# Optimization experiments

Hardware: AMD Instinct MI355X
Metric: run time of the kernel (lower is better)

The kernel has to match this reference:

```python
import jax, jax.numpy as jnp
import numpy as np
import math

EMBED_DIM = 1024
N_HEADS = 16
HEAD_DIM = EMBED_DIM // N_HEADS
B, N = 2, 2048


def setup_inputs() -> dict:
    key = jax.random.key(0)
    k1, k2, k3 = jax.random.split(key, 3)
    x = jax.random.normal(k1, (B, N, EMBED_DIM), dtype=jnp.float32)
    # Per-head Linear(D, 3*head_dim), stacked over heads. PyTorch Linear init scale ~1/sqrt(fan_in).
    bound = 1.0 / math.sqrt(EMBED_DIM)
    Wkqv = jax.random.uniform(k2, (N_HEADS, EMBED_DIM, 3 * HEAD_DIM), dtype=jnp.float32, minval=-bound, maxval=bound)
    bkqv = jax.random.uniform(k3, (N_HEADS, 3 * HEAD_DIM), dtype=jnp.float32, minval=-bound, maxval=bound)
    return {"x": x, "Wkqv": Wkqv, "bkqv": bkqv}


def reference(x, Wkqv, bkqv):
    Bx, Nx, D = x.shape
    hd = Wkqv.shape[-1] // 3
    # all heads at once: [B, H, N, 3*hd]
    proj = jnp.einsum('bnd,hdf->bhnf', x, Wkqv) + bkqv[None, :, None, :]
    # torch.split order in the original is (k, q, v)
    k, q, v = jnp.split(proj, 3, axis=-1)
    # scores = q @ k^T / sqrt(head_dim)   [B, H, N, N]
    scores = jnp.einsum('bhqd,bhkd->bhqk', q, k) / math.sqrt(hd)
    causal = jnp.tril(jnp.ones((Nx, Nx), dtype=bool))
    scores = jnp.where(causal[None, None, :, :], scores, -jnp.inf)
    attn = jax.nn.softmax(scores, axis=-1)
    out = jnp.einsum('bhqk,bhkd->bhqd', attn, v)  # [B, H, N, hd]
    # concat heads -> [B, N, D]  (forward() passes no out_matrix, so no output projection)
    return out.transpose(0, 2, 1, 3).reshape(Bx, Nx, D)
```

## Files before the change

### kernel.cpp

```cpp
#include <hip/hip_runtime.h>
#include <math.h>

typedef float f32x4 __attribute__((ext_vector_type(4)));
typedef __bf16 bf16x8 __attribute__((ext_vector_type(8)));
typedef __bf16 bf16x4 __attribute__((ext_vector_type(4)));

#define MFMA16(a, b, c) __builtin_amdgcn_mfma_f32_16x16x32_bf16((a), (b), (c), 0, 0, 0)

constexpr int Bsz = 2, Nseq = 2048, Dm = 1024, Hh = 16, HDim = 64, F3 = 192;
constexpr int Mrows = Bsz * Nseq;
constexpr int NC = Hh * F3;
constexpr float QSCALE = 0.125f * 1.4426950408889634f;

__device__ inline void load_lds16(const void* g, void* l) {
    __builtin_amdgcn_global_load_lds((const __attribute__((address_space(1))) void*)g,
                                     (__attribute__((address_space(3))) void*)l, 16, 0, 0);
}

#define FENCE asm volatile("" ::: "memory")
#define BARRIER do { FENCE; __builtin_amdgcn_s_barrier(); FENCE; } while (0)


__global__ __launch_bounds__(256) void conv_xw_kernel(const float* __restrict__ x,
                                                      __bf16* __restrict__ xb,
                                                      const float* __restrict__ w,
                                                      __bf16* __restrict__ wt) {
    __shared__ __bf16 tile[32][66];
    if (blockIdx.x < 2048) {
        int i = blockIdx.x * 256 + threadIdx.x;
        const float4* xv = reinterpret_cast<const float4*>(x);
        float4 a = xv[2 * i];
        float4 b = xv[2 * i + 1];
        bf16x8 o = {(__bf16)a.x, (__bf16)a.y, (__bf16)a.z, (__bf16)a.w,
                    (__bf16)b.x, (__bf16)b.y, (__bf16)b.z, (__bf16)b.w};
        *reinterpret_cast<bf16x8*>(xb + 8 * i) = o;
    } else {
        int id = blockIdx.x - 2048;
        int h = id / 96, rem = id % 96;
        int d0 = (rem & 31) * 32, c0 = (rem >> 5) * 64;
        for (int i = threadIdx.x; i < 32 * 64; i += 256) {
            int di = i >> 6, cj = i & 63;
            tile[di][cj] = (__bf16)w[(size_t)(h * Dm + d0 + di) * F3 + c0 + cj];
        }
        __syncthreads();
        for (int i = threadIdx.x; i < 32 * 64; i += 256) {
            int ci = i >> 5, dj = i & 31;
            wt[(size_t)(h * F3 + c0 + ci) * Dm + d0 + dj] = tile[dj][ci];
        }
    }
}

__global__ __launch_bounds__(256) void conv_w_kernel(const float* __restrict__ w,
                                                     __bf16* __restrict__ wt) {
    __shared__ __bf16 tile[32][66];
    int h = blockIdx.z, d0 = blockIdx.x * 32, c0 = blockIdx.y * 64;
    for (int i = threadIdx.x; i < 32 * 64; i += 256) {
        int di = i >> 6, cj = i & 63;
        tile[di][cj] = (__bf16)w[(size_t)(h * Dm + d0 + di) * F3 + c0 + cj];
    }
    __syncthreads();
    for (int i = threadIdx.x; i < 32 * 64; i += 256) {
        int ci = i >> 5, dj = i & 31;
        wt[(size_t)(h * F3 + c0 + ci) * Dm + d0 + dj] = tile[dj][ci];
    }
}

__global__ __launch_bounds__(512, 2) void gemm_proj(const __bf16* __restrict__ xb,
                                                    const __bf16* __restrict__ wt,
                                                    const float* __restrict__ bias,
                                                    __bf16* __restrict__ kbuf,
                                                    __bf16* __restrict__ qbuf,
                                                    __bf16* __restrict__ vt) {
    __shared__ __align__(16) __bf16 Ab[2][256 * 64];
    __shared__ __align__(16) __bf16 Bb[2][192 * 64];

    int flat = blockIdx.x;
    int swz = (flat & 7) * 32 + (flat >> 3);
    int bm = swz >> 4, bn = swz & 15;
    int r0 = bm * 256, n0 = bn * 192;

    int w = threadIdx.x >> 6, lane = threadIdx.x & 63;
    int col = lane & 15, quad = lane >> 4;
    int wm = w >> 2, wn = w & 3;

    f32x4 acc[8][3] = {};

    int rl = lane >> 3;
    int cg = ((lane & 7) ^ rl) * 8;

    auto stage = [&](int t, int s) {
#pragma unroll
        for (int i = 0; i < 4; i++) {
            int rowb = w * 32 + i * 8;
            load_lds16(xb + (size_t)(r0 + rowb + rl) * Dm + t * 64 + cg,
                       &Ab[s][rowb * 64]);
        }
#pragma unroll
        for (int i = 0; i < 3; i++) {
            int rowb = w * 24 + i * 8;
            load_lds16(wt + (size_t)(n0 + rowb + rl) * Dm + t * 64 + cg,
                       &Bb[s][rowb * 64]);
        }
    };

    stage(0, 0);
    stage(1, 1);

    for (int j = 0; j < 16; j++) {
        int s = j & 1;
        if (j < 15) asm volatile("s_waitcnt vmcnt(7)" ::: "memory");
        else        asm volatile("s_waitcnt vmcnt(0)" ::: "memory");
        BARRIER;

#pragma unroll
        for (int ks = 0; ks < 2; ks++) {
            int cq = ks * 4 + quad;
            bf16x8 af[8], bfr[3];
#pragma unroll
            for (int mt = 0; mt < 8; mt++) {
                int row = wm * 128 + mt * 16 + col;
                af[mt] = *reinterpret_cast<const bf16x8*>(
                    &Ab[s][row * 64 + ((cq ^ (row & 7)) * 8)]);
            }
#pragma unroll
            for (int nt = 0; nt < 3; nt++) {
                int row = wn * 48 + nt * 16 + col;
                bfr[nt] = *reinterpret_cast<const bf16x8*>(
                    &Bb[s][row * 64 + ((cq ^ (row & 7)) * 8)]);
            }
            __builtin_amdgcn_s_setprio(1);
#pragma unroll
            for (int mt = 0; mt < 8; mt++)
#pragma unroll
                for (int nt = 0; nt < 3; nt++)
                    acc[mt][nt] = MFMA16(af[mt], bfr[nt], acc[mt][nt]);
            __builtin_amdgcn_s_setprio(0);
        }

        BARRIER;
        if (j + 2 < 16) stage(j + 2, s);
    }

#pragma unroll
    for (int nt = 0; nt < 3; nt++) {
        int g = n0 + wn * 48 + nt * 16 + col;
        int h = g / F3, c = g - h * F3;
        float bv = bias[g];
        bool isq = (c >= 64 && c < 128), isv = (c >= 128);
        int cd = c & 63;
#pragma unroll
        for (int mt = 0; mt < 8; mt++) {
#pragma unroll
            for (int rg = 0; rg < 4; rg++) {
                int r = r0 + wm * 128 + mt * 16 + quad * 4 + rg;
                int b = r >> 11, n = r & (Nseq - 1);
                float v = acc[mt][nt][rg] + bv;
                if (isq) v *= QSCALE;
                size_t bh = (size_t)(b * Hh + h);
                if (isv) {
                    int np = (n & ~63) | ((n & 15) << 2) | ((n >> 4) & 3);
                    vt[(bh * HDim + cd) * Nseq + np] = (__bf16)v;
                } else {
                    ((isq) ? qbuf : kbuf)[(bh * Nseq + n) * HDim + cd] = (__bf16)v;
                }
            }
        }
    }
}

__global__ __launch_bounds__(256) void proj_small(const float* __restrict__ x,
                                                  const __bf16* __restrict__ wt,
                                                  const float* __restrict__ bias,
                                                  __bf16* __restrict__ kbuf,
                                                  __bf16* __restrict__ qbuf,
                                                  __bf16* __restrict__ vt) {
    int h = blockIdx.y;
    int wave = threadIdx.x >> 6, lane = threadIdx.x & 63;
    int col = lane & 15, quad = lane >> 4;
    int r0 = blockIdx.x * 128 + wave * 32;

    f32x4 acc[12][2] = {};
    const float* xr0 = x + (size_t)(r0 + col) * Dm + quad * 8;
    const float* xr1 = xr0 + 16 * Dm;
    const __bf16* wbase = wt + (size_t)(h * F3 + col) * Dm + quad * 8;

    for (int k0 = 0; k0 < Dm; k0 += 32) {
        float4 a0lo = *reinterpret_cast<const float4*>(xr0 + k0);
        float4 a0hi = *reinterpret_cast<const float4*>(xr0 + k0 + 4);
        float4 a1lo = *reinterpret_cast<const float4*>(xr1 + k0);
        float4 a1hi = *reinterpret_cast<const float4*>(xr1 + k0 + 4);
        bf16x8 a0 = {(__bf16)a0lo.x, (__bf16)a0lo.y, (__bf16)a0lo.z, (__bf16)a0lo.w,
                     (__bf16)a0hi.x, (__bf16)a0hi.y, (__bf16)a0hi.z, (__bf16)a0hi.w};
        bf16x8 a1 = {(__bf16)a1lo.x, (__bf16)a1lo.y, (__bf16)a1lo.z, (__bf16)a1lo.w,
                     (__bf16)a1hi.x, (__bf16)a1hi.y, (__bf16)a1hi.z, (__bf16)a1hi.w};
#pragma unroll
        for (int ct = 0; ct < 12; ct++) {
            bf16x8 bf = *reinterpret_cast<const bf16x8*>(wbase + ct * 16 * Dm + k0);
            acc[ct][0] = MFMA16(a0, bf, acc[ct][0]);
            acc[ct][1] = MFMA16(a1, bf, acc[ct][1]);
        }
    }
#pragma unroll
    for (int ct = 0; ct < 12; ct++) {
        int c = ct * 16 + col;
        float bv = bias[h * F3 + c];
        int cd = c & 63;
        bool isq = (c >= 64 && c < 128), isv = (c >= 128);
#pragma unroll
        for (int rt = 0; rt < 2; rt++) {
#pragma unroll
            for (int rg = 0; rg < 4; rg++) {
                int r = r0 + rt * 16 + quad * 4 + rg;
                int b = r >> 11, n = r & (Nseq - 1);
                float v = acc[ct][rt][rg] + bv;
                if (isq) v *= QSCALE;
                size_t bh = (size_t)(b * Hh + h);
                if (isv) {
                    int np = (n & ~63) | ((n & 15) << 2) | ((n >> 4) & 3);
                    vt[(bh * HDim + cd) * Nseq + np] = (__bf16)v;
                } else {
                    ((isq) ? qbuf : kbuf)[(bh * Nseq + n) * HDim + cd] = (__bf16)v;
                }
            }
        }
    }
}

__global__ __launch_bounds__(256) void attn_kernel(const __bf16* __restrict__ qbuf,
                                                   const __bf16* __restrict__ kbuf,
                                                   const __bf16* __restrict__ vt,
                                                   float* __restrict__ out) {
    __shared__ __align__(16) __bf16 Kb[2][64 * 64];
    __shared__ __align__(16) __bf16 Vb[2][64 * 64];
    __shared__ __align__(16) __bf16 plds[4][16 * 64];
    int bh = blockIdx.x;
    int b = bh >> 4, h = bh & 15;
    int tile = 31 - blockIdx.y;
    int wave = threadIdx.x >> 6, lane = threadIdx.x & 63;
    int col = lane & 15, quad = lane >> 4;
    int q0 = tile * 64 + wave * 16;

    const __bf16* qbase = qbuf + (size_t)bh * Nseq * HDim;
    const __bf16* kbase = kbuf + (size_t)bh * Nseq * HDim;
    const __bf16* vbase = vt + (size_t)bh * HDim * Nseq;

    bf16x8 aq0 = *reinterpret_cast<const bf16x8*>(qbase + (q0 + col) * HDim + quad * 8);
    bf16x8 aq1 = *reinterpret_cast<const bf16x8*>(qbase + (q0 + col) * HDim + quad * 8 + 32);

    const bf16x8 vone = {(__bf16)1.f, (__bf16)1.f, (__bf16)1.f, (__bf16)1.f,
                         (__bf16)1.f, (__bf16)1.f, (__bf16)1.f, (__bf16)1.f};

    f32x4 o[4] = {};
    f32x4 ls = {};

    int mb = tile * 64;
    int loop_end = mb + 64;

    int rl = lane >> 3;
    int srow0 = wave * 16 + rl;
    int srow1 = wave * 16 + 8 + rl;
    int sc = (lane & 7) ^ rl;
    const __bf16* ksrc0 = kbase + srow0 * HDim + sc * 8;
    const __bf16* ksrc1 = kbase + srow1 * HDim + sc * 8;
    const __bf16* vsrc0 = vbase + (size_t)srow0 * Nseq + sc * 8;
    const __bf16* vsrc1 = vbase + (size_t)srow1 * Nseq + sc * 8;
    int d0 = wave * 1024, d1 = wave * 1024 + 512;

    int sw0 = ((quad ^ (col & 7)) * 8);
    int sw1 = (((quad + 4) ^ (col & 7)) * 8);

    int pr0 = col * 64 + ((quad ^ (col & 7)) << 3);
    int pr1 = col * 64 + (((quad + 4) ^ (col & 7)) << 3);

    load_lds16(ksrc0, &Kb[0][d0]);
    load_lds16(ksrc1, &Kb[0][d1]);
    load_lds16(vsrc0, &Vb[0][d0]);
    load_lds16(vsrc1, &Vb[0][d1]);
    FENCE;

    int s = 0;
    for (int kb = 0; kb < loop_end; kb += 64) {
        asm volatile("s_waitcnt vmcnt(0)" ::: "memory");
        BARRIER;
        int nkb = kb + 64;
        load_lds16(ksrc0 + nkb * HDim, &Kb[s ^ 1][d0]);
        load_lds16(ksrc1 + nkb * HDim, &Kb[s ^ 1][d1]);
        load_lds16(vsrc0 + nkb, &Vb[s ^ 1][d0]);
        load_lds16(vsrc1 + nkb, &Vb[s ^ 1][d1]);

        bool masked = (kb == mb);
        const __bf16* Kcur = Kb[s];
        const __bf16* Vcur = Vb[s];
        f32x4 z = {};
        f32x4 sc4[4];
#pragma unroll
        for (int g = 0; g < 4; g++) {
            const __bf16* krow = Kcur + (col + 16 * g) * 64;
            bf16x8 k0 = *reinterpret_cast<const bf16x8*>(krow + sw0);
            bf16x8 k1 = *reinterpret_cast<const bf16x8*>(krow + sw1);
            sc4[g] = MFMA16(aq0, k0, z);
            sc4[g] = MFMA16(aq1, k1, sc4[g]);
        }
        if (masked) {
#pragma unroll
            for (int r = 0; r < 4; r++) {
                int row = quad * 4 + r;
                int qi = q0 + row;
                bf16x4 pk;
#pragma unroll
                for (int g = 0; g < 4; g++) {
                    float p = (kb + col + 16 * g <= qi) ? exp2f(sc4[g][r]) : 0.f;
                    pk[g] = (__bf16)p;
                }
                *reinterpret_cast<bf16x4*>(
                    &plds[wave][row * 64 + ((col ^ ((row & 7) << 1)) << 2)]) = pk;
            }
        } else {
#pragma unroll
            for (int r = 0; r < 4; r++) {
                int row = quad * 4 + r;
                bf16x4 pk;
#pragma unroll
                for (int g = 0; g < 4; g++) pk[g] = (__bf16)exp2f(sc4[g][r]);
                *reinterpret_cast<bf16x4*>(
                    &plds[wave][row * 64 + ((col ^ ((row & 7) << 1)) << 2)]) = pk;
            }
        }
        bf16x8 pa0 = *reinterpret_cast<const bf16x8*>(&plds[wave][pr0]);
        bf16x8 pa1 = *reinterpret_cast<const bf16x8*>(&plds[wave][pr1]);
        ls = MFMA16(pa0, vone, ls);
        ls = MFMA16(pa1, vone, ls);
#pragma unroll
        for (int nt = 0; nt < 4; nt++) {
            const __bf16* vrow = Vcur + (col + 16 * nt) * 64;
            bf16x8 v0 = *reinterpret_cast<const bf16x8*>(vrow + sw0);
            bf16x8 v1 = *reinterpret_cast<const bf16x8*>(vrow + sw1);
            o[nt] = MFMA16(pa0, v0, o[nt]);
            o[nt] = MFMA16(pa1, v1, o[nt]);
        }
        s ^= 1;
    }

    float linv[4];
#pragma unroll
    for (int r = 0; r < 4; r++) linv[r] = 1.f / ls[r];
#pragma unroll
    for (int nt = 0; nt < 4; nt++) {
#pragma unroll
        for (int r = 0; r < 4; r++) {
            int qi = q0 + quad * 4 + r;
            out[((size_t)(b * Nseq + qi)) * Dm + h * HDim + nt * 16 + col] = o[nt][r] * linv[r];
        }
    }
}

extern "C" void kernel_launch(void* const* d_in, const int* in_sizes, int n_in,
                              void* d_out, int out_size, void* d_ws, size_t ws_size,
                              hipStream_t stream) {
    const float* x = nullptr;
    const float* w = nullptr;
    const float* bias = nullptr;
    for (int i = 0; i < n_in; i++) {
        if (in_sizes[i] == Mrows * Dm) x = (const float*)d_in[i];
        else if (in_sizes[i] == Hh * Dm * F3) w = (const float*)d_in[i];
        else if (in_sizes[i] == Hh * F3) bias = (const float*)d_in[i];
    }
    float* outp = (float*)d_out;

    char* ws = (char*)d_ws;
    __bf16* wt = (__bf16*)(ws);
    __bf16* kbuf = (__bf16*)(ws + 6291456);
    __bf16* qbuf = (__bf16*)(ws + 6291456 + 8388608);
    __bf16* vt = (__bf16*)(ws + 6291456 + 2 * 8388608);
    __bf16* xb = (__bf16*)(ws + 6291456 + 3 * 8388608);

    if (ws_size >= (size_t)(6291456 + 4 * 8388608)) {
        conv_xw_kernel<<<3584, 256, 0, stream>>>(x, xb, w, wt);
        gemm_proj<<<dim3((Mrows / 256) * (NC / 192)), 512, 0, stream>>>(xb, wt, bias, kbuf, qbuf, vt);
    } else {
        conv_w_kernel<<<dim3(Dm / 32, F3 / 64, Hh), 256, 0, stream>>>(w, wt);
        proj_small<<<dim3(Mrows / 128, Hh), 256, 0, stream>>>(x, wt, bias, kbuf, qbuf, vt);
    }
    attn_kernel<<<dim3(32, 32), 256, 0, stream>>>(qbuf, kbuf, vt, outp);
}
```

Measured before the change: 155.8 us.

## Process two query tiles per attention block to reuse K/V fragments

Each attention workgroup now handles two adjacent 64-row query tiles (128 rows), sharing each K/V LDS load and register fragment load between both tiles. The grid is halved to 32x16 blocks. This cuts global-to-LDS traffic and LDS reads per query row. The cost is more registers per thread, which can lower occupancy, plus fewer and longer blocks, which may worsen load balance across CUs on the causal triangle. It also adds a branch for the first tile's inactive final iteration.

Result: slower. 175.2 us (+12.4%).

```diff
diff --git a/kernel.cpp b/kernel.cpp
--- a/kernel.cpp
+++ b/kernel.cpp
@@ -235,26 +235,30 @@
     __shared__ __align__(16) __bf16 plds[4][16 * 64];
     int bh = blockIdx.x;
     int b = bh >> 4, h = bh & 15;
-    int tile = 31 - blockIdx.y;
+    int T = 15 - blockIdx.y;
     int wave = threadIdx.x >> 6, lane = threadIdx.x & 63;
     int col = lane & 15, quad = lane >> 4;
-    int q0 = tile * 64 + wave * 16;
+    int q0a = T * 128 + wave * 16;
+    int q0b = q0a + 64;
 
     const __bf16* qbase = qbuf + (size_t)bh * Nseq * HDim;
     const __bf16* kbase = kbuf + (size_t)bh * Nseq * HDim;
     const __bf16* vbase = vt + (size_t)bh * HDim * Nseq;
 
-    bf16x8 aq0 = *reinterpret_cast<const bf16x8*>(qbase + (q0 + col) * HDim + quad * 8);
-    bf16x8 aq1 = *reinterpret_cast<const bf16x8*>(qbase + (q0 + col) * HDim + quad * 8 + 32);
+    bf16x8 aq0a = *reinterpret_cast<const bf16x8*>(qbase + (q0a + col) * HDim + quad * 8);
+    bf16x8 aq1a = *reinterpret_cast<const bf16x8*>(qbase + (q0a + col) * HDim + quad * 8 + 32);
+    bf16x8 aq0b = *reinterpret_cast<const bf16x8*>(qbase + (q0b + col) * HDim + quad * 8);
+    bf16x8 aq1b = *reinterpret_cast<const bf16x8*>(qbase + (q0b + col) * HDim + quad * 8 + 32);
 
     const bf16x8 vone = {(__bf16)1.f, (__bf16)1.f, (__bf16)1.f, (__bf16)1.f,
                          (__bf16)1.f, (__bf16)1.f, (__bf16)1.f, (__bf16)1.f};
 
-    f32x4 o[4] = {};
-    f32x4 ls = {};
-
-    int mb = tile * 64;
-    int loop_end = mb + 64;
+    f32x4 oA[4] = {}, oB[4] = {};
+    f32x4 lsA = {}, lsB = {};
+
+    int mba = T * 128;
+    int mbb = T * 128 + 64;
+    int loop_end = T * 128 + 128;
 
     int rl = lane >> 3;
     int srow0 = wave * 16 + rl;
@@ -288,28 +292,87 @@
         load_lds16(vsrc0 + nkb, &Vb[s ^ 1][d0]);
         load_lds16(vsrc1 + nkb, &Vb[s ^ 1][d1]);
 
-        bool masked = (kb == mb);
         const __bf16* Kcur = Kb[s];
         const __bf16* Vcur = Vb[s];
-        f32x4 z = {};
-        f32x4 sc4[4];
+        bool actA = (kb <= mba);
+        bool mA = (kb == mba), mB = (kb == mbb);
+
+        bf16x8 kf0[4], kf1[4];
 #pragma unroll
         for (int g = 0; g < 4; g++) {
             const __bf16* krow = Kcur + (col + 16 * g) * 64;
-            bf16x8 k0 = *reinterpret_cast<const bf16x8*>(krow + sw0);
-            bf16x8 k1 = *reinterpret_cast<const bf16x8*>(krow + sw1);
-            sc4[g] = MFMA16(aq0, k0, z);
-            sc4[g] = MFMA16(aq1, k1, sc4[g]);
-        }
-        if (masked) {
+            kf0[g] = *reinterpret_cast<const bf16x8*>(krow + sw0);
+            kf1[g] = *reinterpret_cast<const bf16x8*>(krow + sw1);
+        }
+        f32x4 z = {};
+        f32x4 sa[4], sb[4];
+#pragma unroll
+        for (int g = 0; g < 4; g++) {
+            sb[g] = MFMA16(aq0b, kf0[g], z);
+            sb[g] = MFMA16(aq1b, kf1[g], sb[g]);
+        }
+        if (actA) {
+#pragma unroll
+            for (int g = 0; g < 4; g++) {
+                sa[g] = MFMA16(aq0a, kf0[g], z);
+                sa[g] = MFMA16(aq1a, kf1[g], sa[g]);
+            }
+        }
+
+        bf16x8 vf0[4], vf1[4];
+#pragma unroll
+        for (int nt = 0; nt < 4; nt++) {
+            const __bf16* vrow = Vcur + (col + 16 * nt) * 64;
+            vf0[nt] = *reinterpret_cast<const bf16x8*>(vrow + sw0);
+            vf1[nt] = *reinterpret_cast<const bf16x8*>(vrow + sw1);
+        }
+
+        if (actA) {
+            if (mA) {
+#pragma unroll
+                for (int r = 0; r < 4; r++) {
+                    int row = quad * 4 + r;
+                    int qi = q0a + row;
+                    bf16x4 pk;
+#pragma unroll
+                    for (int g = 0; g < 4; g++) {
+                        float p = (kb + col + 16 * g <= qi) ? exp2f(sa[g][r]) : 0.f;
+                        pk[g] = (__bf16)p;
+                    }
+                    *reinterpret_cast<bf16x4*>(
+                        &plds[wave][row * 64 + ((col ^ ((row & 7) << 1)) << 2)]) = pk;
+                }
+            } else {
+#pragma unroll
+                for (int r = 0; r < 4; r++) {
+                    int row = quad * 4 + r;
+                    bf16x4 pk;
+#pragma unroll
+                    for (int g = 0; g < 4; g++) pk[g] = (__bf16)exp2f(sa[g][r]);
+                    *reinterpret_cast<bf16x4*>(
+                        &plds[wave][row * 64 + ((col ^ ((row & 7) << 1)) << 2)]) = pk;
+                }
+            }
+            bf16x8 pa0 = *reinterpret_cast<const bf16x8*>(&plds[wave][pr0]);
+            bf16x8 pa1 = *reinterpret_cast<const bf16x8*>(&plds[wave][pr1]);
+            lsA = MFMA16(pa0, vone, lsA);
+            lsA = MFMA16(pa1, vone, lsA);
+#pragma unroll
+            for (int nt = 0; nt < 4; nt++) {
+                oA[nt] = MFMA16(pa0, vf0[nt], oA[nt]);
+                oA[nt] = MFMA16(pa1, vf1[nt], oA[nt]);
+            }
+        }
+
+        if (mB) {
 #pragma unroll
             for (int r = 0; r < 4; r++) {
                 int row = quad * 4 + r;
-                int qi = q0 + row;
+                int qi = q0b + row;
                 bf16x4 pk;
 #pragma unroll
                 for (int g = 0; g < 4; g++) {
-                    float p = (kb + col + 16 * g <= qi) ? exp2f(sc4[g][r]) : 0.f;
+                    float p = (kb + col + 16 * g <= qi) ? exp2f(sb[g][r]) : 0.f;
                     pk[g] = (__bf16)p;
                 }
                 *reinterpret_cast<bf16x4*>(
@@ -321,35 +384,39 @@
                 int row = quad * 4 + r;
                 bf16x4 pk;
 #pragma unroll
-                for (int g = 0; g < 4; g++) pk[g] = (__bf16)exp2f(sc4[g][r]);
+                for (int g = 0; g < 4; g++) pk[g] = (__bf16)exp2f(sb[g][r]);
                 *reinterpret_cast<bf16x4*>(
                     &plds[wave][row * 64 + ((col ^ ((row & 7) << 1)) << 2)]) = pk;
             }
         }
-        bf16x8 pa0 = *reinterpret_cast<const bf16x8*>(&plds[wave][pr0]);
-        bf16x8 pa1 = *reinterpret_cast<const bf16x8*>(&plds[wave][pr1]);
-        ls = MFMA16(pa0, vone, ls);
-        ls = MFMA16(pa1, vone, ls);
-#pragma unroll
-        for (int nt = 0; nt < 4; nt++) {
-            const __bf16* vrow = Vcur + (col + 16 * nt) * 64;
-            bf16x8 v0 = *reinterpret_cast<const bf16x8*>(vrow + sw0);
-            bf16x8 v1 = *reinterpret_cast<const bf16x8*>(vrow + sw1);
-            o[nt] = MFMA16(pa0, v0, o[nt]);
-            o[nt] = MFMA16(pa1, v1, o[nt]);
+        {
+            bf16x8 pb0 = *reinterpret_cast<const bf16x8*>(&plds[wave][pr0]);
+            bf16x8 pb1 = *reinterpret_cast<const bf16x8*>(&plds[wave][pr1]);
+            lsB = MFMA16(pb0, vone, lsB);
+            lsB = MFMA16(pb1, vone, lsB);
+#pragma unroll
+            for (int nt = 0; nt < 4; nt++) {
+                oB[nt] = MFMA16(pb0, vf0[nt], oB[nt]);
+                oB[nt] = MFMA16(pb1, vf1[nt], oB[nt]);
+            }
         }
         s ^= 1;
     }
 
-    float linv[4];
-#pragma unroll
-    for (int r = 0; r < 4; r++) linv[r] = 1.f / ls[r];
+    float linvA[4], linvB[4];
+#pragma unroll
+    for (int r = 0; r < 4; r++) {
+        linvA[r] = 1.f / lsA[r];
+        linvB[r] = 1.f / lsB[r];
+    }
 #pragma unroll
     for (int nt = 0; nt < 4; nt++) {
 #pragma unroll
         for (int r = 0; r < 4; r++) {
-            int qi = q0 + quad * 4 + r;
-            out[((size_t)(b * Nseq + qi)) * Dm + h * HDim + nt * 16 + col] = o[nt][r] * linv[r];
+            int qia = q0a + quad * 4 + r;
+            int qib = q0b + quad * 4 + r;
+            out[((size_t)(b * Nseq + qia)) * Dm + h * HDim + nt * 16 + col] = oA[nt][r] * linvA[r];
+            out[((size_t)(b * Nseq + qib)) * Dm + h * HDim + nt * 16 + col] = oB[nt][r] * linvB[r];
         }
     }
 }
@@ -381,5 +448,5 @@
         conv_w_kernel<<<dim3(Dm / 32, F3 / 64, Hh), 256, 0, stream>>>(w, wt);
         proj_small<<<dim3(Mrows / 128, Hh), 256, 0, stream>>>(x, wt, bias, kbuf, qbuf, vt);
     }
-    attn_kernel<<<dim3(32, 32), 256, 0, stream>>>(qbuf, kbuf, vt, outp);
-}
+    attn_kernel<<<dim3(32, 16), 256, 0, stream>>>(qbuf, kbuf, vt, outp);
+}
```
